# Performance work log

Hardware: AMD Instinct MI355X
Metric: run time of the kernel (lower is better)

## Reference

```python
import jax, jax.numpy as jnp
import numpy as np

EPS = 1e-12  # F.normalize eps


def _l2norm_spatial(x):
    # F.normalize(x, p=2, dim=(2,3)): divide by max(||x||_2 over HxW, eps)
    n = jnp.sqrt(jnp.sum(x * x, axis=(2, 3), keepdims=True))
    return x / jnp.maximum(n, EPS)


def _cscr_forward(rgb, ir):
    C = rgb.shape[1]
    # channel average pooling (cap) and channel max pooling (cmp)
    rgb_cap = jnp.mean(rgb, axis=1, keepdims=True)
    rgb_cmp = jnp.max(rgb, axis=1, keepdims=True)
    ir_cap = jnp.mean(ir, axis=1, keepdims=True)
    ir_cmp = jnp.max(ir, axis=1, keepdims=True)
    # cp = cat([cap,cmp]) summed across modalities; sa = max(cp[:,0::2], cp[:,1::2])
    sa = jnp.maximum(rgb_cap + ir_cap, rgb_cmp + ir_cmp)  # [B,1,H,W]
    sa_sig = jax.nn.sigmoid(sa)

    # cosine similarity of each channel with the (sigmoid'd) spatial attention map
    sa_n = _l2norm_spatial(sa_sig)
    sim_rgb = jnp.sum(sa_n * _l2norm_spatial(rgb), axis=(2, 3))  # [B,C]
    sim_ir = jnp.sum(sa_n * _l2norm_spatial(ir), axis=(2, 3))    # [B,C]

    # sort channels by similarity ascending and gather
    ord_rgb = jnp.argsort(sim_rgb, axis=1)
    ord_ir = jnp.argsort(sim_ir, axis=1)
    sorted_rgb = jnp.take_along_axis(rgb, ord_rgb[:, :, None, None], axis=1)
    sorted_ir = jnp.take_along_axis(ir, ord_ir[:, :, None, None], axis=1)

    # split point = max over batch of #positive similarities (scalar per stream)
    n_rgb = jnp.max(jnp.sum(sim_rgb > 0, axis=1))
    n_ir = jnp.max(jnp.sum(sim_ir > 0, axis=1))

    # When C_rgb == C_ir, torch's equalize_channel_lengths_positive pads the
    # stream with the SMALLER positive count with one extra channel
    # max(sorted_rgb[:, :1], sorted_ir[:, :1]) (the strided slice [::extra] of
    # the first `extra` channels collapses to channel 0), and the subsequent
    # negative truncation drops that stream's last (most positive) channel.
    # The stream with the larger positive count comes out as its full sorted
    # channels. We express that shape-statically with a shifted gather + where.
    extra_fea = jnp.maximum(sorted_rgb[:, :1], sorted_ir[:, :1])  # [B,1,H,W]
    idx = jnp.arange(C)

    def reassemble(sorted_x, n_self, n_other):
        g = jnp.where(idx <= n_self, idx, idx - 1)          # gather with shift after insertion point
        shifted = jnp.take(sorted_x, g, axis=1)             # [B,C,H,W]
        inserted = jnp.where((idx == n_self)[None, :, None, None], extra_fea, shifted)
        return jnp.where(n_other > n_self, inserted, sorted_x)

    rgb_cs = reassemble(sorted_rgb, n_rgb, n_ir)
    ir_cs = reassemble(sorted_ir, n_ir, n_rgb)

    # final spatial-attention gating
    return rgb_cs * sa_sig, ir_cs * sa_sig


def setup_inputs() -> dict:
    key = jax.random.key(0)
    k1, k2 = jax.random.split(key)
    B, C, H, W = 32, 256, 56, 56
    rgb = jax.random.normal(k1, (B, C, H, W), dtype=jnp.float32)
    ir = jax.random.normal(k2, (B, C, H, W), dtype=jnp.float32)
    return {"rgb": rgb, "ir": ir}


def reference(rgb, ir):
    return _cscr_forward(rgb, ir)
```

## Files before the change

### kernel.cpp

```cpp
#include <hip/hip_runtime.h>
#include <math.h>


#define CDIM   256
#define HWDIM  3136
#define CHW    (CDIM * HWDIM)
#define PAIRS  1568

typedef unsigned short u16;
typedef unsigned int   u32;

__device__ __forceinline__ float bf2f(u32 u) { return __uint_as_float(u << 16); }
__device__ __forceinline__ u16  f2bf(float f) {
    u32 x = __float_as_uint(f);
    return (u16)((x + 0x7FFFu + ((x >> 16) & 1u)) >> 16);
}
__device__ __forceinline__ u32 pack2(u32 u, float s0, float s1) {
    float a0 = __uint_as_float(u << 16);
    float a1 = __uint_as_float(u & 0xFFFF0000u);
    u32 lo = f2bf(a0 * s0), hi = f2bf(a1 * s1);
    return lo | (hi << 16);
}
__device__ __forceinline__ u32 maxpack2(u32 u, u32 w, float s0, float s1) {
    float a0 = __uint_as_float(u << 16), a1 = __uint_as_float(u & 0xFFFF0000u);
    float b0 = __uint_as_float(w << 16), b1 = __uint_as_float(w & 0xFFFF0000u);
    u32 lo = f2bf(fmaxf(a0, b0) * s0), hi = f2bf(fmaxf(a1, b1) * s1);
    return lo | (hi << 16);
}

__global__ void k_detect(const u16* __restrict__ rgb, int* __restrict__ flag) {
    __shared__ int cs;
    if (threadIdx.x == 0) cs = 0;
    __syncthreads();
    int w = 0;
    for (int i = threadIdx.x; i < 8192; i += 256) {
        u16 u = rgb[i];
        int e = (u >> 7) & 0xFF;
        float v = bf2f((u32)u);
        if (e == 0xFF || fabsf(v) > 1e3f) w++;
    }
    atomicAdd(&cs, w);
    __syncthreads();
    if (threadIdx.x == 0) flag[0] = (cs > 256) ? 1 : 0;
}

__global__ __launch_bounds__(256) void k_sa(const void* __restrict__ rgb_,
                                            const void* __restrict__ ir_,
                                            const int* __restrict__ flag,
                                            float* __restrict__ sa32) {
    int b  = blockIdx.y;
    int g  = threadIdx.x >> 6;
    int pl = blockIdx.x * 64 + (threadIdx.x & 63);
    bool act = pl < PAIRS;
    int md = flag[0];

    double s0 = 0.0, s1 = 0.0;
    float m0r = -INFINITY, m1r = -INFINITY, m0i = -INFINITY, m1i = -INFINITY;
    if (act) {
        size_t base = (size_t)b * (CHW / 2) + pl;
        if (md == 0) {
            const u32* R = (const u32*)rgb_;
            const u32* I = (const u32*)ir_;
            for (int c = g; c < CDIM; c += 4) {
                u32 wr = R[base + (size_t)c * PAIRS];
                u32 wi = I[base + (size_t)c * PAIRS];
                float r0 = bf2f(wr & 0xFFFFu), r1 = bf2f(wr >> 16);
                float i0 = bf2f(wi & 0xFFFFu), i1 = bf2f(wi >> 16);
                s0 += (double)r0 + (double)i0;
                s1 += (double)r1 + (double)i1;
                m0r = fmaxf(m0r, r0); m1r = fmaxf(m1r, r1);
                m0i = fmaxf(m0i, i0); m1i = fmaxf(m1i, i1);
            }
        } else {
            const float2* R = (const float2*)rgb_;
            const float2* I = (const float2*)ir_;
            for (int c = g; c < CDIM; c += 4) {
                float2 vr = R[base + (size_t)c * PAIRS];
                float2 vi = I[base + (size_t)c * PAIRS];
                s0 += (double)vr.x + (double)vi.x;
                s1 += (double)vr.y + (double)vi.y;
                m0r = fmaxf(m0r, vr.x); m1r = fmaxf(m1r, vr.y);
                m0i = fmaxf(m0i, vi.x); m1i = fmaxf(m1i, vi.y);
            }
        }
    }
    __shared__ double sh_s0[256], sh_s1[256];
    __shared__ float sh_m0r[256], sh_m1r[256], sh_m0i[256], sh_m1i[256];
    int t = threadIdx.x;
    sh_s0[t] = s0; sh_s1[t] = s1;
    sh_m0r[t] = m0r; sh_m1r[t] = m1r; sh_m0i[t] = m0i; sh_m1i[t] = m1i;
    __syncthreads();
    if (g == 0 && act) {
        #pragma unroll
        for (int k = 1; k < 4; ++k) {
            int t2 = t + 64 * k;
            s0 += sh_s0[t2]; s1 += sh_s1[t2];
            m0r = fmaxf(m0r, sh_m0r[t2]); m1r = fmaxf(m1r, sh_m1r[t2]);
            m0i = fmaxf(m0i, sh_m0i[t2]); m1i = fmaxf(m1i, sh_m1i[t2]);
        }
        double sa0 = fmax(s0 * (1.0 / 256.0), (double)m0r + (double)m0i);
        double sa1 = fmax(s1 * (1.0 / 256.0), (double)m1r + (double)m1i);
        size_t o = (size_t)b * HWDIM + 2 * pl;
        sa32[o]     = (float)(1.0 / (1.0 + exp(-sa0)));
        sa32[o + 1] = (float)(1.0 / (1.0 + exp(-sa1)));
    }
}

__global__ __launch_bounds__(256) void k_sim(const void* __restrict__ rgb_,
                                             const void* __restrict__ ir_,
                                             const int* __restrict__ flag,
                                             const float* __restrict__ sa32,
                                             double* __restrict__ sims) {
    __shared__ float s_sa[HWDIM];
    int p0 = blockIdx.x * 4;
    int b  = (p0 >> 8) & 31;
    for (int i = threadIdx.x; i < HWDIM; i += 256)
        s_sa[i] = sa32[(size_t)b * HWDIM + i];
    __syncthreads();

    int wid = threadIdx.x >> 6, lane = threadIdx.x & 63;
    int p = p0 + wid;
    int stream = p >> 13;
    int md = flag[0];
    size_t base = (size_t)(p & 8191) * PAIRS;

    double ss = 0.0, dot = 0.0;
    if (md == 0) {
        const u32* x = (const u32*)(stream ? ir_ : rgb_);
        for (int j = lane; j < PAIRS; j += 64) {
            u32 w = x[base + j];
            double v0 = (double)bf2f(w & 0xFFFFu), v1 = (double)bf2f(w >> 16);
            ss  = fma(v0, v0, fma(v1, v1, ss));
            dot = fma((double)s_sa[2 * j], v0, fma((double)s_sa[2 * j + 1], v1, dot));
        }
    } else {
        const float2* x = (const float2*)(stream ? ir_ : rgb_);
        for (int j = lane; j < PAIRS; j += 64) {
            float2 w = x[base + j];
            double v0 = (double)w.x, v1 = (double)w.y;
            ss  = fma(v0, v0, fma(v1, v1, ss));
            dot = fma((double)s_sa[2 * j], v0, fma((double)s_sa[2 * j + 1], v1, dot));
        }
    }
    #pragma unroll
    for (int off = 32; off >= 1; off >>= 1) {
        ss  += __shfl_xor(ss,  off, 64);
        dot += __shfl_xor(dot, off, 64);
    }
    if (lane == 0) {
        double nrm = sqrt(ss);
        if (nrm < 1e-12) nrm = 1e-12;
        sims[p] = dot / nrm;
    }
}

__global__ __launch_bounds__(256) void k_sort(const double* __restrict__ sims,
                                              int* __restrict__ ord,
                                              int* __restrict__ cnt) {
    __shared__ double s[256];
    __shared__ int csum;
    int sb = blockIdx.x;
    int c  = threadIdx.x;
    double v = sims[sb * 256 + c];
    if (isnan(v)) v = -INFINITY;
    s[c] = v;
    if (c == 0) csum = 0;
    __syncthreads();
    int rank = 0;
    #pragma unroll 8
    for (int j = 0; j < 256; ++j) {
        double u = s[j];
        rank += (u < v) || (u == v && j < c);
    }
    ord[sb * 256 + rank] = c;
    unsigned long long m = __ballot(v > 0.0);
    if ((c & 63) == 0) atomicAdd(&csum, (int)__popcll(m));
    __syncthreads();
    if (c == 0) cnt[sb] = csum;
}

__global__ void k_nmax(const int* __restrict__ cnt, int* __restrict__ nmax) {
    if (threadIdx.x == 0) {
        int n0 = 0, n1 = 0;
        for (int b = 0; b < 32; ++b) {
            n0 = max(n0, cnt[b]);
            n1 = max(n1, cnt[32 + b]);
        }
        nmax[0] = n0; nmax[1] = n1;
    }
}

__global__ __launch_bounds__(256) void k_gather(const void* __restrict__ rgb_,
                                                const void* __restrict__ ir_,
                                                const int* __restrict__ flag,
                                                const float* __restrict__ sa32,
                                                const int* __restrict__ ord,
                                                const int* __restrict__ nmax,
                                                void* __restrict__ out_) {
    int sb = blockIdx.x;
    int stream = sb >> 13;
    int b  = (sb >> 8) & 31;
    int co = sb & 255;
    int md = flag[0];
    int n_self  = nmax[stream];
    int n_other = nmax[1 - stream];
    bool insert  = n_other > n_self;
    bool special = insert && (co == n_self);
    int obase = sb & ~255;

    const float*  sig = sa32 + (size_t)b * HWDIM;
    const float4* sg  = (const float4*)sig;

    if (!special) {
        int ci = co;
        if (insert && co > n_self) ci = co - 1;
        int src = ord[obase + ci] & 255;
        size_t pb = (size_t)(b * 256 + src) * HWDIM;
        if (md == 0) {
            const u16* x = stream ? (const u16*)ir_ : (const u16*)rgb_;
            const uint4* xin = (const uint4*)(x + pb);
            uint4* o = (uint4*)((u16*)out_ + (size_t)sb * HWDIM);
            for (int i = threadIdx.x; i < 392; i += 256) {
                uint4 u = xin[i];
                float4 s0 = sg[2 * i], s1 = sg[2 * i + 1];
                uint4 r;
                r.x = pack2(u.x, s0.x, s0.y);
                r.y = pack2(u.y, s0.z, s0.w);
                r.z = pack2(u.z, s1.x, s1.y);
                r.w = pack2(u.w, s1.z, s1.w);
                o[i] = r;
            }
        } else {
            const float* x = stream ? (const float*)ir_ : (const float*)rgb_;
            const float4* xin = (const float4*)(x + pb);
            float4* o = (float4*)((float*)out_ + (size_t)sb * HWDIM);
            for (int i = threadIdx.x; i < 784; i += 256) {
                float4 v = xin[i], s = sg[i];
                o[i] = make_float4(v.x * s.x, v.y * s.y, v.z * s.z, v.w * s.w);
            }
        }
    } else {
        int src_r = ord[b * 256] & 255;
        int src_i = ord[8192 + b * 256] & 255;
        size_t pr = (size_t)(b * 256 + src_r) * HWDIM;
        size_t pi = (size_t)(b * 256 + src_i) * HWDIM;
        if (md == 0) {
            const uint4* xr = (const uint4*)((const u16*)rgb_ + pr);
            const uint4* xi = (const uint4*)((const u16*)ir_  + pi);
            uint4* o = (uint4*)((u16*)out_ + (size_t)sb * HWDIM);
            for (int i = threadIdx.x; i < 392; i += 256) {
                uint4 u = xr[i], w = xi[i];
                float4 s0 = sg[2 * i], s1 = sg[2 * i + 1];
                uint4 r;
                r.x = maxpack2(u.x, w.x, s0.x, s0.y);
                r.y = maxpack2(u.y, w.y, s0.z, s0.w);
                r.z = maxpack2(u.z, w.z, s1.x, s1.y);
                r.w = maxpack2(u.w, w.w, s1.z, s1.w);
                o[i] = r;
            }
        } else {
            const float4* xr = (const float4*)((const float*)rgb_ + pr);
            const float4* xi = (const float4*)((const float*)ir_  + pi);
            float4* o = (float4*)((float*)out_ + (size_t)sb * HWDIM);
            for (int i = threadIdx.x; i < 784; i += 256) {
                float4 u = xr[i], w = xi[i], s = sg[i];
                o[i] = make_float4(fmaxf(u.x, w.x) * s.x, fmaxf(u.y, w.y) * s.y,
                                   fmaxf(u.z, w.z) * s.z, fmaxf(u.w, w.w) * s.w);
            }
        }
    }
}

extern "C" void kernel_launch(void* const* d_in, const int* in_sizes, int n_in,
                              void* d_out, int out_size, void* d_ws, size_t ws_size,
                              hipStream_t stream) {
    const void* rgb = d_in[0];
    const void* ir  = d_in[1];

    char* ws = (char*)d_ws;
    int*    flg  = (int*)   ws;
    float*  sa32 = (float*) (ws + 1024);
    double* sims = (double*)(ws + 402432);
    int*    ord  = (int*)   (ws + 533504);
    int*    cnt  = (int*)   (ws + 599040);
    int*    nmx  = (int*)   (ws + 599296);

    k_detect<<<1,            256, 0, stream>>>((const u16*)rgb, flg);
    k_sa    <<<dim3(25, 32), 256, 0, stream>>>(rgb, ir, flg, sa32);
    k_sim   <<<4096,         256, 0, stream>>>(rgb, ir, flg, sa32, sims);
    k_sort  <<<64,           256, 0, stream>>>(sims, ord, cnt);
    k_nmax  <<<1,             64, 0, stream>>>(cnt, nmx);
    k_gather<<<16384,        256, 0, stream>>>(rgb, ir, flg, sa32, ord, nmx, d_out);
}
```

Baseline: 442.4 us.

## Fuse detect and nmax kernels, widen loads to four elements in sa and sim

The dtype-detection pass is folded into every k_sa block, and the batch-max reduction moves into k_sort through an atomicMax on nmx, which k_sa zeroes first. That removes two tiny launches from the chain. k_sa and k_sim now process four spatial elements per thread with float4 loads (or paired u32 loads for bf16), which halves the k_sa grid and shortens the loop trip counts. The cost is redundant detection work in each k_sa block and more registers per thread.

Measured after the change: 430.1 us. 1.03x faster.

```diff
diff --git a/kernel.cpp b/kernel.cpp
--- a/kernel.cpp
+++ b/kernel.cpp
@@ -6,6 +6,7 @@
 #define HWDIM  3136
 #define CHW    (CDIM * HWDIM)
 #define PAIRS  1568
+#define QUADS  784
 
 typedef unsigned short u16;
 typedef unsigned int   u32;
@@ -28,118 +29,165 @@
     return lo | (hi << 16);
 }
 
-__global__ void k_detect(const u16* __restrict__ rgb, int* __restrict__ flag) {
-    __shared__ int cs;
-    if (threadIdx.x == 0) cs = 0;
-    __syncthreads();
-    int w = 0;
-    for (int i = threadIdx.x; i < 8192; i += 256) {
-        u16 u = rgb[i];
-        int e = (u >> 7) & 0xFF;
-        float v = bf2f((u32)u);
-        if (e == 0xFF || fabsf(v) > 1e3f) w++;
-    }
-    atomicAdd(&cs, w);
-    __syncthreads();
-    if (threadIdx.x == 0) flag[0] = (cs > 256) ? 1 : 0;
-}
-
 __global__ __launch_bounds__(256) void k_sa(const void* __restrict__ rgb_,
                                             const void* __restrict__ ir_,
-                                            const int* __restrict__ flag,
-                                            float* __restrict__ sa32) {
+                                            int* __restrict__ flg,
+                                            float* __restrict__ sa32,
+                                            int* __restrict__ nmx) {
+    __shared__ int s_det;
+    if (threadIdx.x == 0) s_det = 0;
+    __syncthreads();
+    {
+        const u16* r16 = (const u16*)rgb_;
+        int w = 0;
+        for (int i = threadIdx.x; i < 8192; i += 256) {
+            u16 u = r16[i];
+            int e = (u >> 7) & 0xFF;
+            float v = bf2f((u32)u);
+            if (e == 0xFF || fabsf(v) > 1e3f) w++;
+        }
+        atomicAdd(&s_det, w);
+    }
+    __syncthreads();
+    int md = (s_det > 256) ? 1 : 0;
+    if (blockIdx.x == 0 && blockIdx.y == 0 && threadIdx.x == 0) {
+        flg[0] = md;
+        nmx[0] = 0; nmx[1] = 0;
+    }
+
     int b  = blockIdx.y;
     int g  = threadIdx.x >> 6;
-    int pl = blockIdx.x * 64 + (threadIdx.x & 63);
-    bool act = pl < PAIRS;
-    int md = flag[0];
-
-    double s0 = 0.0, s1 = 0.0;
-    float m0r = -INFINITY, m1r = -INFINITY, m0i = -INFINITY, m1i = -INFINITY;
+    int ql = blockIdx.x * 64 + (threadIdx.x & 63);
+    bool act = ql < QUADS;
+
+    double s0 = 0.0, s1 = 0.0, s2 = 0.0, s3 = 0.0;
+    float m0r = -INFINITY, m1r = -INFINITY, m2r = -INFINITY, m3r = -INFINITY;
+    float m0i = -INFINITY, m1i = -INFINITY, m2i = -INFINITY, m3i = -INFINITY;
+
     if (act) {
-        size_t base = (size_t)b * (CHW / 2) + pl;
-        if (md == 0) {
+        if (md == 1) {
+            const float4* R = (const float4*)rgb_;
+            const float4* I = (const float4*)ir_;
+            size_t bq = (size_t)b * (CHW / 4) + ql;
+            #pragma unroll 2
+            for (int c = g; c < CDIM; c += 4) {
+                float4 r = R[bq + (size_t)c * QUADS];
+                float4 i = I[bq + (size_t)c * QUADS];
+                s0 += (double)r.x + (double)i.x;
+                s1 += (double)r.y + (double)i.y;
+                s2 += (double)r.z + (double)i.z;
+                s3 += (double)r.w + (double)i.w;
+                m0r = fmaxf(m0r, r.x); m1r = fmaxf(m1r, r.y);
+                m2r = fmaxf(m2r, r.z); m3r = fmaxf(m3r, r.w);
+                m0i = fmaxf(m0i, i.x); m1i = fmaxf(m1i, i.y);
+                m2i = fmaxf(m2i, i.z); m3i = fmaxf(m3i, i.w);
+            }
+        } else {
             const u32* R = (const u32*)rgb_;
             const u32* I = (const u32*)ir_;
+            size_t bw = (size_t)b * (CHW / 2) + 2 * (size_t)ql;
+            #pragma unroll 2
             for (int c = g; c < CDIM; c += 4) {
-                u32 wr = R[base + (size_t)c * PAIRS];
-                u32 wi = I[base + (size_t)c * PAIRS];
-                float r0 = bf2f(wr & 0xFFFFu), r1 = bf2f(wr >> 16);
-                float i0 = bf2f(wi & 0xFFFFu), i1 = bf2f(wi >> 16);
+                size_t o = bw + (size_t)c * PAIRS;
+                u32 wr0 = R[o], wr1 = R[o + 1];
+                u32 wi0 = I[o], wi1 = I[o + 1];
+                float r0 = bf2f(wr0 & 0xFFFFu), r1 = bf2f(wr0 >> 16);
+                float r2 = bf2f(wr1 & 0xFFFFu), r3 = bf2f(wr1 >> 16);
+                float i0 = bf2f(wi0 & 0xFFFFu), i1 = bf2f(wi0 >> 16);
+                float i2 = bf2f(wi1 & 0xFFFFu), i3 = bf2f(wi1 >> 16);
                 s0 += (double)r0 + (double)i0;
                 s1 += (double)r1 + (double)i1;
+                s2 += (double)r2 + (double)i2;
+                s3 += (double)r3 + (double)i3;
                 m0r = fmaxf(m0r, r0); m1r = fmaxf(m1r, r1);
+                m2r = fmaxf(m2r, r2); m3r = fmaxf(m3r, r3);
                 m0i = fmaxf(m0i, i0); m1i = fmaxf(m1i, i1);
-            }
-        } else {
-            const float2* R = (const float2*)rgb_;
-            const float2* I = (const float2*)ir_;
-            for (int c = g; c < CDIM; c += 4) {
-                float2 vr = R[base + (size_t)c * PAIRS];
-                float2 vi = I[base + (size_t)c * PAIRS];
-                s0 += (double)vr.x + (double)vi.x;
-                s1 += (double)vr.y + (double)vi.y;
-                m0r = fmaxf(m0r, vr.x); m1r = fmaxf(m1r, vr.y);
-                m0i = fmaxf(m0i, vi.x); m1i = fmaxf(m1i, vi.y);
-            }
-        }
-    }
-    __shared__ double sh_s0[256], sh_s1[256];
-    __shared__ float sh_m0r[256], sh_m1r[256], sh_m0i[256], sh_m1i[256];
+                m2i = fmaxf(m2i, i2); m3i = fmaxf(m3i, i3);
+            }
+        }
+    }
+
+    __shared__ double shs[4][256];
+    __shared__ float  shr[4][256];
+    __shared__ float  shi[4][256];
     int t = threadIdx.x;
-    sh_s0[t] = s0; sh_s1[t] = s1;
-    sh_m0r[t] = m0r; sh_m1r[t] = m1r; sh_m0i[t] = m0i; sh_m1i[t] = m1i;
+    shs[0][t] = s0; shs[1][t] = s1; shs[2][t] = s2; shs[3][t] = s3;
+    shr[0][t] = m0r; shr[1][t] = m1r; shr[2][t] = m2r; shr[3][t] = m3r;
+    shi[0][t] = m0i; shi[1][t] = m1i; shi[2][t] = m2i; shi[3][t] = m3i;
     __syncthreads();
     if (g == 0 && act) {
         #pragma unroll
         for (int k = 1; k < 4; ++k) {
             int t2 = t + 64 * k;
-            s0 += sh_s0[t2]; s1 += sh_s1[t2];
-            m0r = fmaxf(m0r, sh_m0r[t2]); m1r = fmaxf(m1r, sh_m1r[t2]);
-            m0i = fmaxf(m0i, sh_m0i[t2]); m1i = fmaxf(m1i, sh_m1i[t2]);
+            s0 += shs[0][t2]; s1 += shs[1][t2];
+            s2 += shs[2][t2]; s3 += shs[3][t2];
+            m0r = fmaxf(m0r, shr[0][t2]); m1r = fmaxf(m1r, shr[1][t2]);
+            m2r = fmaxf(m2r, shr[2][t2]); m3r = fmaxf(m3r, shr[3][t2]);
+            m0i = fmaxf(m0i, shi[0][t2]); m1i = fmaxf(m1i, shi[1][t2]);
+            m2i = fmaxf(m2i, shi[2][t2]); m3i = fmaxf(m3i, shi[3][t2]);
         }
         double sa0 = fmax(s0 * (1.0 / 256.0), (double)m0r + (double)m0i);
         double sa1 = fmax(s1 * (1.0 / 256.0), (double)m1r + (double)m1i);
-        size_t o = (size_t)b * HWDIM + 2 * pl;
-        sa32[o]     = (float)(1.0 / (1.0 + exp(-sa0)));
-        sa32[o + 1] = (float)(1.0 / (1.0 + exp(-sa1)));
+        double sa2 = fmax(s2 * (1.0 / 256.0), (double)m2r + (double)m2i);
+        double sa3 = fmax(s3 * (1.0 / 256.0), (double)m3r + (double)m3i);
+        float4 ov;
+        ov.x = (float)(1.0 / (1.0 + exp(-sa0)));
+        ov.y = (float)(1.0 / (1.0 + exp(-sa1)));
+        ov.z = (float)(1.0 / (1.0 + exp(-sa2)));
+        ov.w = (float)(1.0 / (1.0 + exp(-sa3)));
+        *(float4*)&sa32[(size_t)b * HWDIM + 4 * (size_t)ql] = ov;
     }
 }
 
 __global__ __launch_bounds__(256) void k_sim(const void* __restrict__ rgb_,
                                              const void* __restrict__ ir_,
-                                             const int* __restrict__ flag,
+                                             const int* __restrict__ flg,
                                              const float* __restrict__ sa32,
                                              double* __restrict__ sims) {
     __shared__ float s_sa[HWDIM];
     int p0 = blockIdx.x * 4;
     int b  = (p0 >> 8) & 31;
-    for (int i = threadIdx.x; i < HWDIM; i += 256)
-        s_sa[i] = sa32[(size_t)b * HWDIM + i];
+    {
+        const float4* src = (const float4*)(sa32 + (size_t)b * HWDIM);
+        float4* dst = (float4*)s_sa;
+        for (int i = threadIdx.x; i < QUADS; i += 256) dst[i] = src[i];
+    }
     __syncthreads();
 
     int wid = threadIdx.x >> 6, lane = threadIdx.x & 63;
     int p = p0 + wid;
     int stream = p >> 13;
-    int md = flag[0];
-    size_t base = (size_t)(p & 8191) * PAIRS;
+    int md = flg[0];
+    int plane = p & 8191;
+    const float4* sv = (const float4*)s_sa;
 
     double ss = 0.0, dot = 0.0;
-    if (md == 0) {
-        const u32* x = (const u32*)(stream ? ir_ : rgb_);
-        for (int j = lane; j < PAIRS; j += 64) {
-            u32 w = x[base + j];
-            double v0 = (double)bf2f(w & 0xFFFFu), v1 = (double)bf2f(w >> 16);
-            ss  = fma(v0, v0, fma(v1, v1, ss));
-            dot = fma((double)s_sa[2 * j], v0, fma((double)s_sa[2 * j + 1], v1, dot));
+    if (md == 1) {
+        const float4* x = (const float4*)(stream ? ir_ : rgb_) + (size_t)plane * QUADS;
+        #pragma unroll 2
+        for (int j = lane; j < QUADS; j += 64) {
+            float4 v = x[j];
+            float4 s = sv[j];
+            ss  = fma((double)v.x, (double)v.x,
+                  fma((double)v.y, (double)v.y,
+                  fma((double)v.z, (double)v.z,
+                  fma((double)v.w, (double)v.w, ss))));
+            dot = fma((double)s.x, (double)v.x,
+                  fma((double)s.y, (double)v.y,
+                  fma((double)s.z, (double)v.z,
+                  fma((double)s.w, (double)v.w, dot))));
         }
     } else {
-        const float2* x = (const float2*)(stream ? ir_ : rgb_);
-        for (int j = lane; j < PAIRS; j += 64) {
-            float2 w = x[base + j];
-            double v0 = (double)w.x, v1 = (double)w.y;
-            ss  = fma(v0, v0, fma(v1, v1, ss));
-            dot = fma((double)s_sa[2 * j], v0, fma((double)s_sa[2 * j + 1], v1, dot));
+        const u32* x = (const u32*)(stream ? ir_ : rgb_) + (size_t)plane * PAIRS;
+        #pragma unroll 2
+        for (int j = lane; j < QUADS; j += 64) {
+            u32 w0 = x[2 * j], w1 = x[2 * j + 1];
+            double v0 = (double)bf2f(w0 & 0xFFFFu), v1 = (double)bf2f(w0 >> 16);
+            double v2 = (double)bf2f(w1 & 0xFFFFu), v3 = (double)bf2f(w1 >> 16);
+            float4 s = sv[j];
+            ss  = fma(v0, v0, fma(v1, v1, fma(v2, v2, fma(v3, v3, ss))));
+            dot = fma((double)s.x, v0, fma((double)s.y, v1,
+                  fma((double)s.z, v2, fma((double)s.w, v3, dot))));
         }
     }
     #pragma unroll
@@ -156,7 +204,7 @@
 
 __global__ __launch_bounds__(256) void k_sort(const double* __restrict__ sims,
                                               int* __restrict__ ord,
-                                              int* __restrict__ cnt) {
+                                              int* __restrict__ nmx) {
     __shared__ double s[256];
     __shared__ int csum;
     int sb = blockIdx.x;
@@ -176,23 +224,12 @@
     unsigned long long m = __ballot(v > 0.0);
     if ((c & 63) == 0) atomicAdd(&csum, (int)__popcll(m));
     __syncthreads();
-    if (c == 0) cnt[sb] = csum;
-}
-
-__global__ void k_nmax(const int* __restrict__ cnt, int* __restrict__ nmax) {
-    if (threadIdx.x == 0) {
-        int n0 = 0, n1 = 0;
-        for (int b = 0; b < 32; ++b) {
-            n0 = max(n0, cnt[b]);
-            n1 = max(n1, cnt[32 + b]);
-        }
-        nmax[0] = n0; nmax[1] = n1;
-    }
+    if (c == 0) atomicMax(&nmx[sb >> 5], csum);
 }
 
 __global__ __launch_bounds__(256) void k_gather(const void* __restrict__ rgb_,
                                                 const void* __restrict__ ir_,
-                                                const int* __restrict__ flag,
+                                                const int* __restrict__ flg,
                                                 const float* __restrict__ sa32,
                                                 const int* __restrict__ ord,
                                                 const int* __restrict__ nmax,
@@ -201,7 +238,7 @@
     int stream = sb >> 13;
     int b  = (sb >> 8) & 31;
     int co = sb & 255;
-    int md = flag[0];
+    int md = flg[0];
     int n_self  = nmax[stream];
     int n_other = nmax[1 - stream];
     bool insert  = n_other > n_self;
@@ -282,13 +319,10 @@
     float*  sa32 = (float*) (ws + 1024);
     double* sims = (double*)(ws + 402432);
     int*    ord  = (int*)   (ws + 533504);
-    int*    cnt  = (int*)   (ws + 599040);
     int*    nmx  = (int*)   (ws + 599296);
 
-    k_detect<<<1,            256, 0, stream>>>((const u16*)rgb, flg);
-    k_sa    <<<dim3(25, 32), 256, 0, stream>>>(rgb, ir, flg, sa32);
+    k_sa    <<<dim3(13, 32), 256, 0, stream>>>(rgb, ir, flg, sa32, nmx);
     k_sim   <<<4096,         256, 0, stream>>>(rgb, ir, flg, sa32, sims);
-    k_sort  <<<64,           256, 0, stream>>>(sims, ord, cnt);
-    k_nmax  <<<1,             64, 0, stream>>>(cnt, nmx);
+    k_sort  <<<64,           256, 0, stream>>>(sims, ord, nmx);
     k_gather<<<16384,        256, 0, stream>>>(rgb, ir, flg, sa32, ord, nmx, d_out);
 }
```
